# Performance work log

Hardware: AMD Instinct MI355X
Metric: run time of the kernel (lower is better)

The kernel has to match this reference:

```python
import jax, jax.numpy as jnp
import numpy as np

EPS = 1e-5

def chan_layernorm(x, g):
    # LayerNorm over channel dim (-3), unbiased=False variance, learned scale g [C]
    mean = jnp.mean(x, axis=1, keepdims=True)
    var = jnp.var(x, axis=1, keepdims=True)
    return (x - mean) * jax.lax.rsqrt(var + EPS) * g[None, :, None, None]

def conv1x1(x, w):
    # w: [out_c, in_c]; pointwise conv == channel GEMM
    return jnp.einsum('bchw,oc->bohw', x, w)

def dwconv3x3(x, w):
    # depthwise 3x3, padding=1; w: [C, 1, 3, 3]
    C = x.shape[1]
    return jax.lax.conv_general_dilated(
        x, w, window_strides=(1, 1), padding='SAME',
        feature_group_count=C,
        dimension_numbers=('NCHW', 'OIHW', 'NCHW'))

def setup_inputs() -> dict:
    key = jax.random.key(0)
    ks = jax.random.split(key, 8)
    b, dim, x, y = 8, 512, 64, 64
    s1 = (dim ** -0.5) * 0.5  # modest init scale
    sd = (9 ** -0.5)
    return {
        'fmap': jax.random.normal(ks[0], (b, dim, x, y), jnp.float32),
        'g': jnp.ones((dim,), jnp.float32),
        'wq1': jax.random.normal(ks[1], (dim, dim), jnp.float32) * s1,
        'wq_dw': jax.random.normal(ks[2], (dim, 1, 3, 3), jnp.float32) * sd,
        'wk1': jax.random.normal(ks[3], (dim, dim), jnp.float32) * s1,
        'wk_dw': jax.random.normal(ks[4], (dim, 1, 3, 3), jnp.float32) * sd,
        'wv1': jax.random.normal(ks[5], (dim, dim), jnp.float32) * s1,
        'wv_dw': jax.random.normal(ks[6], (dim, 1, 3, 3), jnp.float32) * sd,
        'w_out': jax.random.normal(ks[7], (dim, dim), jnp.float32) * s1,
    }

def reference(fmap, g, wq1, wq_dw, wk1, wk_dw, wv1, wv_dw, w_out):
    b, dim, x, y = fmap.shape
    h = 8
    d = dim // h
    scale = d ** -0.5

    fm = chan_layernorm(fmap, g)
    q = dwconv3x3(conv1x1(fm, wq1), wq_dw)
    k = dwconv3x3(conv1x1(fm, wk1), wk_dw)
    v = dwconv3x3(conv1x1(fm, wv1), wv_dw)

    # b (h c) x y -> (b h) (x y) c
    def split_heads(t):
        return t.reshape(b, h, d, x * y).transpose(0, 1, 3, 2).reshape(b * h, x * y, d)
    q, k, v = map(split_heads, (q, k, v))

    q = jax.nn.softmax(q, axis=-1) * scale  # softmax over feature dim
    k = jax.nn.softmax(k, axis=-2)          # softmax over token dim

    ctx = jnp.einsum('bnd,bne->bde', k, v)  # [bh, d, d]
    out = jnp.einsum('bnd,bde->bne', q, ctx)  # [bh, n, d]

    # (b h) (x y) d -> b (h d) x y
    out = out.reshape(b, h, x * y, d).transpose(0, 1, 3, 2).reshape(b, h * d, x, y)
    out = jax.nn.silu(out)
    return conv1x1(out, w_out)
```

## Files before the change

### kernel.cpp

```cpp
#include <hip/hip_runtime.h>
#include <hip/hip_bf16.h>

typedef __attribute__((ext_vector_type(8))) short short8;
typedef __attribute__((ext_vector_type(4))) short shortx4;
typedef __attribute__((ext_vector_type(4))) float floatx4;

#define NB 8
#define C 512
#define NSP 4096
#define NHD 8
#define HDD 64

using bf16 = __hip_bfloat16;

__device__ __forceinline__ float b2f(bf16 v) { return __bfloat162float(v); }
__device__ __forceinline__ bf16 f2b(float f) { return __float2bfloat16(f); }
__device__ __forceinline__ float s2f(short s) {
    union { float f; unsigned u; } cv; cv.u = ((unsigned)(unsigned short)s) << 16; return cv.f;
}
__device__ __forceinline__ short f2s(float f) {
    bf16 b = f2b(f); return *reinterpret_cast<short*>(&b);
}

__device__ __forceinline__ void gl2lds16(const bf16* g, bf16* l) {
#if __has_builtin(__builtin_amdgcn_global_load_lds)
    __builtin_amdgcn_global_load_lds(
        (const __attribute__((address_space(1))) unsigned int*)g,
        (__attribute__((address_space(3))) unsigned int*)l, 16, 0, 0);
#else
    *(short8*)l = *(const short8*)g;
#endif
}

__global__ void detect_dtype(const unsigned* __restrict__ g_raw, int* __restrict__ flag) {
    *flag = (g_raw[0] == 0x3F800000u) ? 1 : 0;
}

__global__ __launch_bounds__(256) void prep_w(const void* g, const void* w1q, const void* wdq,
                                              const void* w1k, const void* wdk,
                                              const void* w1v, const void* wdv, const void* w1o,
                                              bf16* gc, bf16* wqkv, bf16* woutc,
                                              bf16* wkdc, bf16* wvdc, bf16* wqdT,
                                              const int* flag) {
    int i = blockIdx.x * 256 + threadIdx.x;
    int f = *flag;
    auto cv = [&](const void* s, int j) -> bf16 {
        return f ? f2b(((const float*)s)[j]) : ((const bf16*)s)[j];
    };
    if (i < C * C) {
        wqkv[i] = cv(w1q, i);
        wqkv[C * C + i] = cv(w1k, i);
        wqkv[2 * C * C + i] = cv(w1v, i);
        woutc[i] = cv(w1o, i);
    }
    if (i < C * 9) {
        int c = i / 9, t = i - c * 9;
        wqdT[t * C + c] = cv(wdq, i);
        wkdc[i] = cv(wdk, i);
        wvdc[i] = cv(wdv, i);
    }
    if (i < C) gc[i] = cv(g, i);
}

__global__ __launch_bounds__(256) void ln_fused(const void* __restrict__ fmap,
                                                const bf16* __restrict__ gc,
                                                bf16* __restrict__ fm,
                                                const int* __restrict__ flag) {
    const int P = 516;
    __shared__ bf16 T[32 * P];
    __shared__ float stat[32][2];
    int b = blockIdx.y;
    int n0 = blockIdx.x * 32;
    int t = threadIdx.x;
    if (*flag) {
        int nq = t & 7;
        int c0 = t >> 3;
        const float* src = (const float*)fmap + (size_t)b * C * NSP + n0 + nq * 4;
#pragma unroll 4
        for (int it = 0; it < 16; ++it) {
            int c = c0 + it * 32;
            float4 v = *(const float4*)(src + (size_t)c * NSP);
            T[(nq * 4 + 0) * P + c] = f2b(v.x);
            T[(nq * 4 + 1) * P + c] = f2b(v.y);
            T[(nq * 4 + 2) * P + c] = f2b(v.z);
            T[(nq * 4 + 3) * P + c] = f2b(v.w);
        }
    } else {
        int nq = t & 3;
        int c0 = t >> 2;
        const bf16* src = (const bf16*)fmap + (size_t)b * C * NSP + n0 + nq * 8;
#pragma unroll 4
        for (int it = 0; it < 8; ++it) {
            int c = c0 + it * 64;
            union { short8 s; short h[8]; } v;
            v.s = *(const short8*)(src + (size_t)c * NSP);
#pragma unroll
            for (int j = 0; j < 8; ++j)
                *(short*)&T[(nq * 8 + j) * P + c] = v.h[j];
        }
    }
    __syncthreads();
    int n = t >> 3, part = t & 7;
    {
        float s = 0.f, sq = 0.f;
        const bf16* row = T + n * P + part * 64;
#pragma unroll
        for (int i = 0; i < 8; ++i) {
            union { short8 v; short h[8]; } u;
            u.v = *(const short8*)(row + i * 8);
#pragma unroll
            for (int j = 0; j < 8; ++j) { float x = s2f(u.h[j]); s += x; sq += x * x; }
        }
#pragma unroll
        for (int off = 1; off < 8; off <<= 1) {
            s += __shfl_xor(s, off, 64);
            sq += __shfl_xor(sq, off, 64);
        }
        if (part == 0) {
            float mean = s * (1.f / C);
            float var = sq * (1.f / C) - mean * mean;
            stat[n][0] = mean;
            stat[n][1] = rsqrtf(var + 1e-5f);
        }
    }
    __syncthreads();
    float mean = stat[n][0], rs = stat[n][1];
    bf16* dst = fm + ((size_t)b * NSP + n0 + n) * C + part * 64;
    const bf16* row = T + n * P + part * 64;
    const bf16* gp = gc + part * 64;
#pragma unroll
    for (int i = 0; i < 8; ++i) {
        union { short8 v; short h[8]; } u, gv, ov;
        u.v = *(const short8*)(row + i * 8);
        gv.v = *(const short8*)(gp + i * 8);
#pragma unroll
        for (int j = 0; j < 8; ++j)
            ov.h[j] = f2s((s2f(u.h[j]) - mean) * rs * s2f(gv.h[j]));
        *(short8*)(dst + i * 8) = ov.v;
    }
}

template <int PHASE>
__global__ __launch_bounds__(256) void gemm_k64(const bf16* __restrict__ X,
                                                const bf16* __restrict__ Wall,
                                                void* __restrict__ O0,
                                                void* __restrict__ O1,
                                                void* __restrict__ O2,
                                                const int* __restrict__ flag) {
    __shared__ bf16 Xs[128 * 64];
    __shared__ bf16 Ws[128 * 64];
    int nbase = blockIdx.x * 128;
    int oy = blockIdx.y;
    int b = blockIdx.z;
    int lane = threadIdx.x & 63, w = threadIdx.x >> 6;
    int wm = w >> 1, wn = w & 1;
    int m16 = lane & 15, q = lane >> 4;
    const bf16* Xb = X + (size_t)b * NSP * C;
    const bf16* Wb = Wall + (size_t)oy * 128 * C;
    int srow = threadIdx.x >> 3;
    int g8 = (threadIdx.x & 7) ^ (srow & 7);
    const bf16* xg = Xb + (size_t)(nbase + srow) * C + g8 * 8;
    const bf16* wg = Wb + (size_t)srow * C + g8 * 8;
    bf16* xl = Xs + threadIdx.x * 8;
    bf16* wl = Ws + threadIdx.x * 8;
    bool AisW = (PHASE == 0) && (oy < 4);
    const bf16* As = AisW ? Ws : Xs;
    const bf16* Bs = AisW ? Xs : Ws;
    int qx = q ^ (m16 & 3);
    int h2 = (m16 >> 2) & 1;

    floatx4 acc[4][4] = {};
    for (int ks = 0; ks < 8; ++ks) {
        int k0 = ks * 64;
        __syncthreads();
#pragma unroll
        for (int i = 0; i < 4; ++i) {
            gl2lds16(xg + (size_t)i * 32 * C + k0, xl + i * 2048);
            gl2lds16(wg + (size_t)i * 32 * C + k0, wl + i * 2048);
        }
        __syncthreads();
#pragma unroll
        for (int half = 0; half < 2; ++half) {
            int ch = ((half ^ h2) * 4 + qx) * 8;
            short8 Af[4], Bf[4];
#pragma unroll
            for (int tt = 0; tt < 4; ++tt) {
                Af[tt] = *(const short8*)(As + (wm * 64 + tt * 16 + m16) * 64 + ch);
                Bf[tt] = *(const short8*)(Bs + (wn * 64 + tt * 16 + m16) * 64 + ch);
            }
#pragma unroll
            for (int mt = 0; mt < 4; ++mt)
#pragma unroll
                for (int nt = 0; nt < 4; ++nt)
                    acc[mt][nt] = __builtin_amdgcn_mfma_f32_16x16x32_bf16(Af[mt], Bf[nt], acc[mt][nt], 0, 0, 0);
        }
    }

    if (PHASE == 0 && oy < 4) {
        bf16* out = (bf16*)O0 + (size_t)b * NSP * C;
#pragma unroll
        for (int nt = 0; nt < 4; ++nt)
#pragma unroll
            for (int mt = 0; mt < 4; ++mt) {
                int n = nbase + wn * 64 + nt * 16 + m16;
                int o = oy * 128 + wm * 64 + mt * 16 + q * 4;
                shortx4 pv;
#pragma unroll
                for (int r = 0; r < 4; ++r) pv[r] = f2s(acc[mt][nt][r]);
                *(shortx4*)(out + (size_t)n * C + o) = pv;
            }
    } else if (PHASE == 0) {
        bf16* out = (bf16*)((oy < 8) ? O1 : O2) + (size_t)b * C * NSP;
        int ob = ((oy - 4) & 3) * 128;
#pragma unroll
        for (int nt = 0; nt < 4; ++nt)
#pragma unroll
            for (int mt = 0; mt < 4; ++mt) {
                int o = ob + wn * 64 + nt * 16 + m16;
                int n = nbase + wm * 64 + mt * 16 + q * 4;
                shortx4 pv;
#pragma unroll
                for (int r = 0; r < 4; ++r) pv[r] = f2s(acc[mt][nt][r]);
                *(shortx4*)(out + (size_t)o * NSP + n) = pv;
            }
    } else {
        int is_f32 = *flag;
        size_t outb = (size_t)b * C * NSP;
#pragma unroll
        for (int nt = 0; nt < 4; ++nt)
#pragma unroll
            for (int mt = 0; mt < 4; ++mt) {
                int o = oy * 128 + wn * 64 + nt * 16 + m16;
                int n = nbase + wm * 64 + mt * 16 + q * 4;
                size_t off = outb + (size_t)o * NSP + n;
                if (is_f32) {
                    *(floatx4*)((float*)O0 + off) = acc[mt][nt];
                } else {
                    shortx4 pv;
#pragma unroll
                    for (int r = 0; r < 4; ++r) pv[r] = f2s(acc[mt][nt][r]);
                    *(shortx4*)((bf16*)O0 + off) = pv;
                }
            }
    }
}

__global__ __launch_bounds__(256) void dwconv_nc8_sm(const bf16* __restrict__ X,
                                                     const bf16* __restrict__ WdT,
                                                     bf16* __restrict__ O) {
    int idx = blockIdx.x * 256 + threadIdx.x;
    int cg = idx & 63;
    int n = (idx >> 6) & (NSP - 1);
    int b = idx >> 18;
    int c0 = cg * 8;
    int y = n >> 6, x = n & 63;
    const bf16* xp = X + (size_t)b * NSP * C + c0;
    union { short8 s; short h[8]; } wv[9];
#pragma unroll
    for (int t = 0; t < 9; ++t) wv[t].s = *(const short8*)(WdT + t * C + c0);
    float acc[8] = {};
#pragma unroll
    for (int ky = 0; ky < 3; ++ky) {
        int yy = y + ky - 1;
        if ((unsigned)yy >= 64u) continue;
#pragma unroll
        for (int kx = 0; kx < 3; ++kx) {
            int xx = x + kx - 1;
            if ((unsigned)xx >= 64u) continue;
            union { short8 s; short h[8]; } iv;
            iv.s = *(const short8*)(xp + (size_t)(yy * 64 + xx) * C);
            int t = ky * 3 + kx;
#pragma unroll
            for (int i = 0; i < 8; ++i)
                acc[i] += s2f(iv.h[i]) * s2f(wv[t].h[i]);
        }
    }
    float mx = acc[0];
#pragma unroll
    for (int i = 1; i < 8; ++i) mx = fmaxf(mx, acc[i]);
#pragma unroll
    for (int off = 1; off < 8; off <<= 1) mx = fmaxf(mx, __shfl_xor(mx, off, 64));
    float e[8], s = 0.f;
#pragma unroll
    for (int i = 0; i < 8; ++i) { e[i] = __expf(acc[i] - mx); s += e[i]; }
#pragma unroll
    for (int off = 1; off < 8; off <<= 1) s += __shfl_xor(s, off, 64);
    float inv = 0.125f / s;
    union { short8 s; short h[8]; } ov;
#pragma unroll
    for (int i = 0; i < 8; ++i) ov.h[i] = f2s(e[i] * inv);
    *(short8*)(O + ((size_t)(b * NSP) + n) * C + c0) = ov.s;
}

__global__ __launch_bounds__(256) void dw_sk(const bf16* __restrict__ X,
                                             const bf16* __restrict__ Wd,
                                             bf16* __restrict__ O) {
    int bc = blockIdx.x;
    int c = bc & (C - 1);
    int t = threadIdx.x;
    int y = t >> 2, x0 = (t & 3) * 16;
    const bf16* xp = X + (size_t)bc * NSP;
    float wv[9];
#pragma unroll
    for (int i = 0; i < 9; ++i) wv[i] = b2f(Wd[c * 9 + i]);
    float a[16];
#pragma unroll
    for (int i = 0; i < 16; ++i) a[i] = 0.f;
#pragma unroll
    for (int ky = 0; ky < 3; ++ky) {
        int yy = y + ky - 1;
        if ((unsigned)yy >= 64u) continue;
        const bf16* rp = xp + yy * 64;
        float v[18];
        v[0] = (x0 > 0) ? b2f(rp[x0 - 1]) : 0.f;
        union { short8 s; short h[8]; } m0, m1;
        m0.s = *(const short8*)(rp + x0);
        m1.s = *(const short8*)(rp + x0 + 8);
#pragma unroll
        for (int j = 0; j < 8; ++j) { v[1 + j] = s2f(m0.h[j]); v[9 + j] = s2f(m1.h[j]); }
        v[17] = (x0 < 48) ? b2f(rp[x0 + 16]) : 0.f;
#pragma unroll
        for (int i = 0; i < 16; ++i)
            a[i] += wv[ky * 3 + 0] * v[i] + wv[ky * 3 + 1] * v[i + 1] + wv[ky * 3 + 2] * v[i + 2];
    }
    float mx = a[0];
#pragma unroll
    for (int i = 1; i < 16; ++i) mx = fmaxf(mx, a[i]);
#pragma unroll
    for (int off = 32; off; off >>= 1) mx = fmaxf(mx, __shfl_xor(mx, off, 64));
    __shared__ float red[4];
    __shared__ float bcv;
    int lane = t & 63, wid = t >> 6;
    if (lane == 0) red[wid] = mx;
    __syncthreads();
    if (t == 0) bcv = fmaxf(fmaxf(red[0], red[1]), fmaxf(red[2], red[3]));
    __syncthreads();
    float M = bcv;
    float s = 0.f;
#pragma unroll
    for (int i = 0; i < 16; ++i) { a[i] = __expf(a[i] - M); s += a[i]; }
#pragma unroll
    for (int off = 32; off; off >>= 1) s += __shfl_xor(s, off, 64);
    __syncthreads();
    if (lane == 0) red[wid] = s;
    __syncthreads();
    if (t == 0) bcv = red[0] + red[1] + red[2] + red[3];
    __syncthreads();
    float inv = 1.f / bcv;
    union { short8 s8; short h[8]; } o0, o1;
#pragma unroll
    for (int j = 0; j < 8; ++j) { o0.h[j] = f2s(a[j] * inv); o1.h[j] = f2s(a[8 + j] * inv); }
    bf16* op = O + (size_t)bc * NSP + y * 64 + x0;
    *(short8*)op = o0.s8;
    *(short8*)(op + 8) = o1.s8;
}

__global__ __launch_bounds__(256) void dwconv_cn8(const bf16* __restrict__ X,
                                                  const bf16* __restrict__ Wd,
                                                  bf16* __restrict__ O) {
    int idx = blockIdx.x * 256 + threadIdx.x;
    int g = idx & 511;
    int bc = idx >> 9;
    int c = bc & (C - 1);
    int y = g >> 3, x0 = (g & 7) * 8;
    const bf16* xp = X + (size_t)bc * NSP;
    float w[9];
#pragma unroll
    for (int t = 0; t < 9; ++t) w[t] = b2f(Wd[c * 9 + t]);
    float acc[8] = {};
#pragma unroll
    for (int ky = 0; ky < 3; ++ky) {
        int yy = y + ky - 1;
        if ((unsigned)yy >= 64u) continue;
        const bf16* rp = xp + yy * 64;
        union { short8 s; short h[8]; } mv;
        mv.s = *(const short8*)(rp + x0);
        float vals[10];
        vals[0] = (x0 > 0) ? b2f(rp[x0 - 1]) : 0.f;
#pragma unroll
        for (int i = 0; i < 8; ++i) vals[i + 1] = s2f(mv.h[i]);
        vals[9] = (x0 < 56) ? b2f(rp[x0 + 8]) : 0.f;
#pragma unroll
        for (int i = 0; i < 8; ++i)
            acc[i] += w[ky * 3 + 0] * vals[i] + w[ky * 3 + 1] * vals[i + 1] + w[ky * 3 + 2] * vals[i + 2];
    }
    union { short8 s; short h[8]; } ov;
#pragma unroll
    for (int i = 0; i < 8; ++i) ov.h[i] = f2s(acc[i]);
    *(short8*)(O + (size_t)bc * NSP + y * 64 + x0) = ov.s;
}

__global__ __launch_bounds__(256) void ctx_mfma(const bf16* __restrict__ K,
                                                const bf16* __restrict__ V,
                                                bf16* __restrict__ ctxb) {
    int bh = blockIdx.y;
    int b = bh >> 3, h = bh & 7;
    int lane = threadIdx.x & 63, w = threadIdx.x >> 6;
    int m16 = lane & 15, q = lane >> 4;
    int ebase = blockIdx.x * 16;
    const bf16* vp = V + ((size_t)b * C + h * 64 + ebase + m16) * NSP + q * 8;
    const bf16* kp = K + ((size_t)b * C + h * 64 + w * 16 + m16) * NSP + q * 8;
    floatx4 acc = {};
#pragma unroll 4
    for (int k0 = 0; k0 < NSP; k0 += 32) {
        short8 a = *(const short8*)(vp + k0);
        short8 bb = *(const short8*)(kp + k0);
        acc = __builtin_amdgcn_mfma_f32_16x16x32_bf16(a, bb, acc, 0, 0, 0);
    }
#pragma unroll
    for (int r = 0; r < 4; ++r) {
        int e = ebase + q * 4 + r;
        int d = w * 16 + m16;
        ctxb[((size_t)bh * 64 + e) * 64 + d] = f2b(acc[r]);
    }
}

__global__ __launch_bounds__(256) void attn_out(const bf16* __restrict__ Q,
                                                const bf16* __restrict__ ctxb,
                                                bf16* __restrict__ O) {
    int nbase = blockIdx.x * 64;
    int bh = blockIdx.y;
    int b = bh >> 3;
    int hb = (bh & 7) * 64;
    int lane = threadIdx.x & 63, w = threadIdx.x >> 6;
    int m16 = lane & 15, q = lane >> 4;
    const bf16* qp = Q + ((size_t)(b * NSP) + nbase + w * 16 + m16) * C + hb + q * 8;
    const bf16* cp = ctxb + ((size_t)bh * 64 + m16) * 64 + q * 8;
    floatx4 acc[4] = {};
#pragma unroll
    for (int ko = 0; ko < 64; ko += 32) {
        short8 a = *(const short8*)(qp + ko);
#pragma unroll
        for (int j = 0; j < 4; ++j) {
            short8 bf = *(const short8*)(cp + (size_t)j * 16 * 64 + ko);
            acc[j] = __builtin_amdgcn_mfma_f32_16x16x32_bf16(a, bf, acc[j], 0, 0, 0);
        }
    }
    bf16* op = O + (size_t)b * NSP * C;
#pragma unroll
    for (int j = 0; j < 4; ++j)
#pragma unroll
        for (int r = 0; r < 4; ++r) {
            int nrow = nbase + w * 16 + q * 4 + r;
            float x = acc[j][r];
            float sv = x / (1.f + __expf(-x));
            op[(size_t)nrow * C + hb + j * 16 + m16] = f2b(sv);
        }
}

extern "C" void kernel_launch(void* const* d_in, const int* in_sizes, int n_in,
                              void* d_out, int out_size, void* d_ws, size_t ws_size,
                              hipStream_t stream) {
    char* ws = (char*)d_ws;
    const size_t TB = (size_t)NB * NSP * C * 2;
    bf16* buf0 = (bf16*)(ws);
    bf16* buf1 = (bf16*)(ws + TB);
    bf16* buf2 = (bf16*)(ws + 2 * TB);
    bf16* buf3 = (bf16*)(ws + 3 * TB);
    char* ext = ws + 4 * TB;
    bf16* ctxb  = (bf16*)(ext);                   ext += 524288;
    bf16* gc    = (bf16*)(ext);                   ext += 4096;
    bf16* wqkv  = (bf16*)(ext);                   ext += 3 * C * C * 2;
    bf16* woutc = (bf16*)(ext);                   ext += C * C * 2;
    bf16* wkdc  = (bf16*)(ext);                   ext += 16384;
    bf16* wvdc  = (bf16*)(ext);                   ext += 16384;
    bf16* wqdT  = (bf16*)(ext);                   ext += 16384;
    int*  flag  = (int*)(ext);                    ext += 4096;

    detect_dtype<<<1, 1, 0, stream>>>((const unsigned*)d_in[1], flag);
    prep_w<<<(C * C + 255) / 256, 256, 0, stream>>>(d_in[1], d_in[2], d_in[3], d_in[4], d_in[5],
                                                    d_in[6], d_in[7], d_in[8],
                                                    gc, wqkv, woutc, wkdc, wvdc, wqdT, flag);

    ln_fused<<<dim3(NSP / 32, NB), 256, 0, stream>>>(d_in[0], gc, buf0, flag);

    gemm_k64<0><<<dim3(NSP / 128, 12, NB), 256, 0, stream>>>(buf0, wqkv, buf1, buf2, buf3, flag);

    dwconv_nc8_sm<<<NB * NSP * 64 / 256, 256, 0, stream>>>(buf1, wqdT, buf0);
    dw_sk<<<NB * C, 256, 0, stream>>>(buf2, wkdc, buf1);
    dwconv_cn8<<<NB * C * 512 / 256, 256, 0, stream>>>(buf3, wvdc, buf2);

    ctx_mfma<<<dim3(4, NB * NHD), 256, 0, stream>>>(buf1, buf2, ctxb);
    attn_out<<<dim3(NSP / 64, NB * NHD), 256, 0, stream>>>(buf0, ctxb, buf3);

    gemm_k64<1><<<dim3(NSP / 128, C / 128, NB), 256, 0, stream>>>(buf3, woutc, d_out, nullptr, nullptr, flag);
}
```

Baseline: 376.0 us.

## Replace GEMM with 256x256 tiles and double-buffered async LDS pipeline

Replaces the 128x128 single-buffered GEMM with a 256x256-tile, 512-thread kernel. It double-buffers A and B tiles in shared memory and interleaves global-to-LDS staging with MFMA phases, using explicit waitcnt, barriers and setprio. The goal is to hide global load latency and raise arithmetic intensity for the QKV and output projections. In exchange it uses 128KB of LDS per block and larger accumulators, so fewer blocks fit per CU, and the grid shrinks, which may leave some CUs idle.

```diff
diff --git a/kernel.cpp b/kernel.cpp
--- a/kernel.cpp
+++ b/kernel.cpp
@@ -141,83 +141,145 @@
 }
 
 template <int PHASE>
-__global__ __launch_bounds__(256) void gemm_k64(const bf16* __restrict__ X,
-                                                const bf16* __restrict__ Wall,
-                                                void* __restrict__ O0,
-                                                void* __restrict__ O1,
-                                                void* __restrict__ O2,
-                                                const int* __restrict__ flag) {
-    __shared__ bf16 Xs[128 * 64];
-    __shared__ bf16 Ws[128 * 64];
-    int nbase = blockIdx.x * 128;
-    int oy = blockIdx.y;
-    int b = blockIdx.z;
-    int lane = threadIdx.x & 63, w = threadIdx.x >> 6;
-    int wm = w >> 1, wn = w & 1;
-    int m16 = lane & 15, q = lane >> 4;
-    const bf16* Xb = X + (size_t)b * NSP * C;
-    const bf16* Wb = Wall + (size_t)oy * 128 * C;
-    int srow = threadIdx.x >> 3;
-    int g8 = (threadIdx.x & 7) ^ (srow & 7);
-    const bf16* xg = Xb + (size_t)(nbase + srow) * C + g8 * 8;
-    const bf16* wg = Wb + (size_t)srow * C + g8 * 8;
-    bf16* xl = Xs + threadIdx.x * 8;
-    bf16* wl = Ws + threadIdx.x * 8;
-    bool AisW = (PHASE == 0) && (oy < 4);
-    const bf16* As = AisW ? Ws : Xs;
-    const bf16* Bs = AisW ? Xs : Ws;
-    int qx = q ^ (m16 & 3);
-    int h2 = (m16 >> 2) & 1;
-
-    floatx4 acc[4][4] = {};
-    for (int ks = 0; ks < 8; ++ks) {
-        int k0 = ks * 64;
-        __syncthreads();
-#pragma unroll
-        for (int i = 0; i < 4; ++i) {
-            gl2lds16(xg + (size_t)i * 32 * C + k0, xl + i * 2048);
-            gl2lds16(wg + (size_t)i * 32 * C + k0, wl + i * 2048);
-        }
-        __syncthreads();
-#pragma unroll
-        for (int half = 0; half < 2; ++half) {
-            int ch = ((half ^ h2) * 4 + qx) * 8;
-            short8 Af[4], Bf[4];
-#pragma unroll
-            for (int tt = 0; tt < 4; ++tt) {
-                Af[tt] = *(const short8*)(As + (wm * 64 + tt * 16 + m16) * 64 + ch);
-                Bf[tt] = *(const short8*)(Bs + (wn * 64 + tt * 16 + m16) * 64 + ch);
-            }
-#pragma unroll
-            for (int mt = 0; mt < 4; ++mt)
-#pragma unroll
-                for (int nt = 0; nt < 4; ++nt)
-                    acc[mt][nt] = __builtin_amdgcn_mfma_f32_16x16x32_bf16(Af[mt], Bf[nt], acc[mt][nt], 0, 0, 0);
-        }
-    }
-
-    if (PHASE == 0 && oy < 4) {
+__global__ __launch_bounds__(512, 2) void gemm256(const bf16* __restrict__ X,
+                                                  const bf16* __restrict__ Wall,
+                                                  void* __restrict__ O0,
+                                                  void* __restrict__ O1,
+                                                  void* __restrict__ O2,
+                                                  const int* __restrict__ flag) {
+    __shared__ __align__(16) bf16 SH[4][256 * 64];
+    bf16* SA0 = SH[0];
+    bf16* SA1 = SH[1];
+    bf16* SB0 = SH[2];
+    bf16* SB1 = SH[3];
+    const int nbase = blockIdx.x * 256;
+    const int obase = blockIdx.y * 256;
+    const int b = blockIdx.z;
+    const int t = threadIdx.x;
+    const int lane = t & 63, w = t >> 6;
+    const int wm = w >> 2, wn = w & 3;
+    const int m16 = lane & 15, q = lane >> 4;
+    const bool AisW = (PHASE == 0) && (obase < 512);
+    const bf16* gX = X + (size_t)b * NSP * C + (size_t)nbase * C;
+    const bf16* gW = Wall + (size_t)obase * C;
+    const bf16* gA = AisW ? gW : gX;
+    const bf16* gB = AisW ? gX : gW;
+
+    const int srow = t >> 3;
+    const int sch = ((t & 7) ^ (srow & 7)) * 8;
+
+    const int rA = wm * 128 + m16;
+    const int rB = wn * 64 + m16;
+    const int cs0 = ((q) ^ (m16 & 7)) * 8;
+    const int cs1 = ((4 + q) ^ (m16 & 7)) * 8;
+
+    floatx4 acc[8][4] = {};
+    short8 Bf[4][2];
+
+#define STAGE(LDS, G, K0, H)                                                   \
+    {                                                                          \
+        const bf16* _s = (G) + (size_t)((H) * 128 + srow) * C + (K0) + sch;    \
+        bf16* _d = (LDS) + (H) * 8192 + t * 8;                                 \
+        gl2lds16(_s, _d);                                                      \
+        gl2lds16(_s + 64 * C, _d + 4096);                                      \
+    }
+
+#define VMW(N)                                                                 \
+    {                                                                          \
+        asm volatile("s_waitcnt vmcnt(" #N ")" ::: "memory");                  \
+        __builtin_amdgcn_sched_barrier(0);                                     \
+    }
+
+#define PH(J, LA, LB, LOADB, STAGE_STMT, WAIT_STMT)                            \
+    {                                                                          \
+        short8 Af0, Af1, Af2, Af3;                                             \
+        if (LOADB) {                                                           \
+            _Pragma("unroll") for (int nt = 0; nt < 4; ++nt) {                 \
+                Bf[nt][0] = *(const short8*)((LB) + (rB + nt * 16) * 64 + cs0);\
+                Bf[nt][1] = *(const short8*)((LB) + (rB + nt * 16) * 64 + cs1);\
+            }                                                                  \
+        }                                                                      \
+        Af0 = *(const short8*)((LA) + (rA + (2 * (J)) * 16) * 64 + cs0);       \
+        Af1 = *(const short8*)((LA) + (rA + (2 * (J)) * 16) * 64 + cs1);       \
+        Af2 = *(const short8*)((LA) + (rA + (2 * (J) + 1) * 16) * 64 + cs0);   \
+        Af3 = *(const short8*)((LA) + (rA + (2 * (J) + 1) * 16) * 64 + cs1);   \
+        STAGE_STMT;                                                            \
+        WAIT_STMT;                                                             \
+        __builtin_amdgcn_sched_barrier(0);                                     \
+        __builtin_amdgcn_s_barrier();                                          \
+        asm volatile("s_waitcnt lgkmcnt(0)" ::: "memory");                     \
+        __builtin_amdgcn_sched_barrier(0);                                     \
+        __builtin_amdgcn_s_setprio(1);                                         \
+        _Pragma("unroll") for (int nt = 0; nt < 4; ++nt) {                     \
+            acc[2 * (J)][nt] = __builtin_amdgcn_mfma_f32_16x16x32_bf16(        \
+                Af0, Bf[nt][0], acc[2 * (J)][nt], 0, 0, 0);                    \
+            acc[2 * (J)][nt] = __builtin_amdgcn_mfma_f32_16x16x32_bf16(        \
+                Af1, Bf[nt][1], acc[2 * (J)][nt], 0, 0, 0);                    \
+            acc[2 * (J) + 1][nt] = __builtin_amdgcn_mfma_f32_16x16x32_bf16(    \
+                Af2, Bf[nt][0], acc[2 * (J) + 1][nt], 0, 0, 0);                \
+            acc[2 * (J) + 1][nt] = __builtin_amdgcn_mfma_f32_16x16x32_bf16(    \
+                Af3, Bf[nt][1], acc[2 * (J) + 1][nt], 0, 0, 0);                \
+        }                                                                      \
+        __builtin_amdgcn_s_setprio(0);                                         \
+        __builtin_amdgcn_sched_barrier(0);                                     \
+        __builtin_amdgcn_s_barrier();                                          \
+    }
+
+    STAGE(SA0, gA, 0, 0);
+    STAGE(SA0, gA, 0, 1);
+    STAGE(SB0, gB, 0, 0);
+    STAGE(SB0, gB, 0, 1);
+    STAGE(SB1, gB, 64, 0);
+    STAGE(SB1, gB, 64, 1);
+    VMW(0);
+    __builtin_amdgcn_s_barrier();
+
+    for (int i = 0; i < 3; ++i) {
+        int kT = i * 128;
+        PH(0, SA0, SB0, true,  STAGE(SA1, gA, kT + 64, 0),  ((void)0));
+        PH(1, SA0, SB0, false, STAGE(SA1, gA, kT + 64, 1),  ((void)0));
+        PH(2, SA0, SB0, false, STAGE(SB0, gB, kT + 128, 0), ((void)0));
+        PH(3, SA0, SB0, false, STAGE(SB0, gB, kT + 128, 1), VMW(4));
+        PH(0, SA1, SB1, true,  STAGE(SA0, gA, kT + 128, 0), ((void)0));
+        PH(1, SA1, SB1, false, STAGE(SA0, gA, kT + 128, 1), ((void)0));
+        PH(2, SA1, SB1, false, STAGE(SB1, gB, kT + 192, 0), ((void)0));
+        PH(3, SA1, SB1, false, STAGE(SB1, gB, kT + 192, 1), VMW(4));
+    }
+    PH(0, SA0, SB0, true,  STAGE(SA1, gA, 448, 0), ((void)0));
+    PH(1, SA0, SB0, false, STAGE(SA1, gA, 448, 1), ((void)0));
+    PH(2, SA0, SB0, false, ((void)0), ((void)0));
+    PH(3, SA0, SB0, false, ((void)0), VMW(0));
+    PH(0, SA1, SB1, true,  ((void)0), ((void)0));
+    PH(1, SA1, SB1, false, ((void)0), ((void)0));
+    PH(2, SA1, SB1, false, ((void)0), ((void)0));
+    PH(3, SA1, SB1, false, ((void)0), ((void)0));
+
+#undef PH
+#undef VMW
+#undef STAGE
+
+    if (PHASE == 0 && AisW) {
         bf16* out = (bf16*)O0 + (size_t)b * NSP * C;
 #pragma unroll
         for (int nt = 0; nt < 4; ++nt)
 #pragma unroll
-            for (int mt = 0; mt < 4; ++mt) {
+            for (int mt = 0; mt < 8; ++mt) {
                 int n = nbase + wn * 64 + nt * 16 + m16;
-                int o = oy * 128 + wm * 64 + mt * 16 + q * 4;
+                int o = obase + wm * 128 + mt * 16 + q * 4;
                 shortx4 pv;
 #pragma unroll
                 for (int r = 0; r < 4; ++r) pv[r] = f2s(acc[mt][nt][r]);
                 *(shortx4*)(out + (size_t)n * C + o) = pv;
             }
     } else if (PHASE == 0) {
-        bf16* out = (bf16*)((oy < 8) ? O1 : O2) + (size_t)b * C * NSP;
-        int ob = ((oy - 4) & 3) * 128;
+        bf16* out = (bf16*)((obase < 1024) ? O1 : O2) + (size_t)b * C * NSP;
+        int ob = obase & 511;
 #pragma unroll
         for (int nt = 0; nt < 4; ++nt)
 #pragma unroll
-            for (int mt = 0; mt < 4; ++mt) {
+            for (int mt = 0; mt < 8; ++mt) {
                 int o = ob + wn * 64 + nt * 16 + m16;
-                int n = nbase + wm * 64 + mt * 16 + q * 4;
+                int n = nbase + wm * 128 + mt * 16 + q * 4;
                 shortx4 pv;
 #pragma unroll
                 for (int r = 0; r < 4; ++r) pv[r] = f2s(acc[mt][nt][r]);
@@ -229,9 +291,9 @@
 #pragma unroll
         for (int nt = 0; nt < 4; ++nt)
 #pragma unroll
-            for (int mt = 0; mt < 4; ++mt) {
-                int o = oy * 128 + wn * 64 + nt * 16 + m16;
-                int n = nbase + wm * 64 + mt * 16 + q * 4;
+            for (int mt = 0; mt < 8; ++mt) {
+                int o = obase + wn * 64 + nt * 16 + m16;
+                int n = nbase + wm * 128 + mt * 16 + q * 4;
                 size_t off = outb + (size_t)o * NSP + n;
                 if (is_f32) {
                     *(floatx4*)((float*)O0 + off) = acc[mt][nt];
@@ -474,7 +536,7 @@
 
     ln_fused<<<dim3(NSP / 32, NB), 256, 0, stream>>>(d_in[0], gc, buf0, flag);
 
-    gemm_k64<0><<<dim3(NSP / 128, 12, NB), 256, 0, stream>>>(buf0, wqkv, buf1, buf2, buf3, flag);
+    gemm256<0><<<dim3(NSP / 256, 6, NB), 512, 0, stream>>>(buf0, wqkv, buf1, buf2, buf3, flag);
 
     dwconv_nc8_sm<<<NB * NSP * 64 / 256, 256, 0, stream>>>(buf1, wqdT, buf0);
     dw_sk<<<NB * C, 256, 0, stream>>>(buf2, wkdc, buf1);
@@ -483,5 +545,5 @@
     ctx_mfma<<<dim3(4, NB * NHD), 256, 0, stream>>>(buf1, buf2, ctxb);
     attn_out<<<dim3(NSP / 64, NB * NHD), 256, 0, stream>>>(buf0, ctxb, buf3);
 
-    gemm_k64<1><<<dim3(NSP / 128, C / 128, NB), 256, 0, stream>>>(buf3, woutc, d_out, nullptr, nullptr, flag);
-}
+    gemm256<1><<<dim3(NSP / 256, C / 256, NB), 512, 0, stream>>>(buf3, woutc, d_out, nullptr, nullptr, flag);
+}
```

New measurement: 378.1 us. Within noise of the previous version (+0.5%).
